# Performance work log

Hardware: AMD Instinct MI355X
Metric: run time of the kernel (lower is better)

Reference implementation:

```python
import jax, jax.numpy as jnp
import numpy as np

NUM_HEADS = 4
HIDDEN = 256
HEAD_DIM = HIDDEN // NUM_HEADS
N_NODES = 8192
N_EDGES = 262144
NEG = -1e9


def setup_inputs() -> dict:
    key = jax.random.key(0)
    ks = jax.random.split(key, 10)
    s = 1.0 / np.sqrt(HIDDEN)
    inp = {
        "node_features": jax.random.normal(ks[0], (N_NODES, HIDDEN), dtype=jnp.float32),
        "Wq": jax.random.uniform(ks[1], (HIDDEN, HIDDEN), jnp.float32, -s, s),
        "bq": jnp.zeros((HIDDEN,), jnp.float32),
        "Wk": jax.random.uniform(ks[2], (HIDDEN, HIDDEN), jnp.float32, -s, s),
        "bk": jnp.zeros((HIDDEN,), jnp.float32),
        "Wv": jax.random.uniform(ks[3], (HIDDEN, HIDDEN), jnp.float32, -s, s),
        "bv": jnp.zeros((HIDDEN,), jnp.float32),
        "Wo": jax.random.uniform(ks[4], (HIDDEN, HIDDEN), jnp.float32, -s, s),
        "bo": jnp.zeros((HIDDEN,), jnp.float32),
        "edge_index": jax.random.randint(ks[5], (2, N_EDGES), 0, N_NODES, dtype=jnp.int64),
    }
    return inp


def reference(node_features, Wq, bq, Wk, bk, Wv, bv, Wo, bo, edge_index):
    N = node_features.shape[0]
    # QKV projections -> [H, N, d]
    q = (node_features @ Wq + bq).reshape(N, NUM_HEADS, HEAD_DIM).transpose(1, 0, 2)
    k = (node_features @ Wk + bk).reshape(N, NUM_HEADS, HEAD_DIM).transpose(1, 0, 2)
    v = (node_features @ Wv + bv).reshape(N, NUM_HEADS, HEAD_DIM).transpose(1, 0, 2)
    # dense scores [H, N, N]
    scores = jnp.einsum('hnd,hmd->hnm', q, k) / jnp.sqrt(jnp.float32(HEAD_DIM))
    mask = jnp.full((N, N), NEG, dtype=jnp.float32).at[edge_index[0], edge_index[1]].set(0.0)
    scores = scores + mask[None, :, :]
    weights = jax.nn.softmax(scores, axis=-1)  # dropout is identity in eval
    context = jnp.einsum('hnm,hmd->hnd', weights, v)
    context = context.transpose(1, 0, 2).reshape(N, HIDDEN)
    return context @ Wo + bo
```

## Files before the change

### kernel.cpp

```cpp
#include <hip/hip_runtime.h>
#include <hip/hip_fp16.h>
#include <stdint.h>

#define NN 8192
#define HID 256
#define NH 4
#define HD 64
#define NE 262144
#define WPR (NN / 32)
#define CAP 128
#define NQKV 768

typedef __attribute__((ext_vector_type(8))) short s16x8;
typedef __attribute__((ext_vector_type(4))) float f32x4;
typedef _Float16 f16x2 __attribute__((ext_vector_type(2)));

__device__ __forceinline__ float fdot2(f16x2 a, f16x2 b, float c) {
#if __has_builtin(__builtin_amdgcn_fdot2)
    return __builtin_amdgcn_fdot2(a, b, c, false);
#else
    return c + (float)a.x * (float)b.x + (float)a.y * (float)b.y;
#endif
}

__device__ __forceinline__ void gload_lds16(const unsigned short* g, unsigned short* l) {
    __builtin_amdgcn_global_load_lds(
        (const __attribute__((address_space(1))) unsigned int*)g,
        (__attribute__((address_space(3))) unsigned int*)l, 16, 0, 0);
}

__global__ __launch_bounds__(256) void zero_kernel(uint4* __restrict__ p)
{
    p[blockIdx.x * 256 + threadIdx.x] = make_uint4(0, 0, 0, 0);
}

__global__ __launch_bounds__(256) void prep_kernel(
    const float* __restrict__ X,
    const float* __restrict__ Wq, const float* __restrict__ Wk,
    const float* __restrict__ Wv, const float* __restrict__ Wo,
    const float* __restrict__ bq, const float* __restrict__ bk,
    const float* __restrict__ bv, const int* __restrict__ ei,
    uint32_t* __restrict__ bitmap, unsigned short* __restrict__ Xh,
    unsigned short* __restrict__ W2Tq, unsigned short* __restrict__ W2To,
    float* __restrict__ biasq)
{
    const int b = blockIdx.x, tid = threadIdx.x;
    if (b < 1024) {
        int e = b * 256 + tid;
        int r = ei[e];
        int c = ei[NE + e];
        atomicOr(&bitmap[(size_t)r * WPR + (c >> 5)], 1u << (c & 31));
    } else if (b < 3072) {
        int i4 = ((b - 1024) * 256 + tid) * 4;
        float4 x = *(const float4*)(X + i4);
        __half2 h0 = __floats2half2_rn(x.x, x.y);
        __half2 h1 = __floats2half2_rn(x.z, x.w);
        uint2 w;
        w.x = *(unsigned*)&h0;
        w.y = *(unsigned*)&h1;
        *(uint2*)(Xh + i4) = w;
    } else {
        int lin = (b - 3072) * 256 + tid;
        int n = lin >> 8, k = lin & 255;
        const float* W; int ns; unsigned short* dst;
        if (n < NQKV) {
            W  = (n < 256) ? Wq : (n < 512) ? Wk : Wv;
            ns = n & 255;
            dst = W2Tq + (size_t)n * HID + k;
            if (k == 0) {
                const float* bsrc = (n < 256) ? bq : (n < 512) ? bk : bv;
                biasq[n] = bsrc[ns];
            }
        } else {
            W = Wo; ns = n - NQKV;
            dst = W2To + (size_t)ns * HID + k;
        }
        __half h = __float2half(W[(size_t)k * HID + ns]);
        *dst = *(unsigned short*)&h;
    }
}

template<int BN, bool HALF_OUT>
__global__ __launch_bounds__(256) void mfma_gemm_kernel(
    const unsigned short* __restrict__ A, const unsigned short* __restrict__ BT,
    const float* __restrict__ bias, void* __restrict__ Cv, int N)
{
    constexpr int NFR = BN / 32;
    __shared__ __align__(16) unsigned short Alds[128 * 32];
    __shared__ __align__(16) unsigned short Blds[BN * 32];

    const int tid  = threadIdx.x;
    const int lane = tid & 63, wave = tid >> 6;
    const int wm = wave >> 1, wn = wave & 1;

    const int nwg = gridDim.x;
    const int orig = blockIdx.x;
    const int q8 = nwg >> 3;
    const int id = (orig & 7) * q8 + (orig >> 3);
    const int m0 = (id & 63) * 128;
    const int n0 = (id >> 6) * BN;

    const int r0 = tid >> 2, cc0 = tid & 3;
    const int r1 = (tid + 256) >> 2, cc1 = (tid + 256) & 3;

    f32x4 acc[4][NFR];
    #pragma unroll
    for (int i = 0; i < 4; ++i)
        #pragma unroll
        for (int j = 0; j < NFR; ++j)
            acc[i][j] = (f32x4){0.f, 0.f, 0.f, 0.f};

    for (int step = 0; step < 8; ++step) {
        const int kk = step * 32;
        __syncthreads();
        gload_lds16(A + (size_t)(m0 + r0) * HID + kk + cc0 * 8, &Alds[tid * 8]);
        gload_lds16(A + (size_t)(m0 + r1) * HID + kk + cc1 * 8, &Alds[(tid + 256) * 8]);
        gload_lds16(BT + (size_t)(n0 + r0) * HID + kk + cc0 * 8, &Blds[tid * 8]);
        if constexpr (BN == 128)
            gload_lds16(BT + (size_t)(n0 + r1) * HID + kk + cc1 * 8, &Blds[(tid + 256) * 8]);
        __syncthreads();

        s16x8 af[4], bfr[NFR];
        #pragma unroll
        for (int i = 0; i < 4; ++i)
            af[i] = *(const s16x8*)&Alds[(wm * 64 + i * 16 + (lane & 15)) * 32 + (lane >> 4) * 8];
        #pragma unroll
        for (int j = 0; j < NFR; ++j)
            bfr[j] = *(const s16x8*)&Blds[(wn * (BN / 2) + j * 16 + (lane & 15)) * 32 + (lane >> 4) * 8];
        #pragma unroll
        for (int i = 0; i < 4; ++i)
            #pragma unroll
            for (int j = 0; j < NFR; ++j)
                acc[i][j] = __builtin_amdgcn_mfma_f32_16x16x32_f16(af[i], bfr[j], acc[i][j], 0, 0, 0);
    }

    #pragma unroll
    for (int i = 0; i < 4; ++i) {
        #pragma unroll
        for (int j = 0; j < NFR; ++j) {
            int gcol = n0 + wn * (BN / 2) + j * 16 + (lane & 15);
            float bb = bias[gcol];
            #pragma unroll
            for (int r = 0; r < 4; ++r) {
                int grow = m0 + wm * 64 + i * 16 + (lane >> 4) * 4 + r;
                float v = acc[i][j][r] + bb;
                if constexpr (HALF_OUT)
                    ((__half*)Cv)[(size_t)grow * N + gcol] = __float2half(v);
                else
                    ((float*)Cv)[(size_t)grow * N + gcol] = v;
            }
        }
    }
}

__global__ __launch_bounds__(256) void build_csr_kernel(
    const uint32_t* __restrict__ bitmap, int* __restrict__ nbr, int* __restrict__ cnt)
{
    const int row = blockIdx.x * 4 + (threadIdx.x >> 6);
    const int lane = threadIdx.x & 63;
    const uint32_t* rp = bitmap + (size_t)row * WPR + lane * 4;
    uint32_t w0 = rp[0], w1 = rp[1], w2 = rp[2], w3 = rp[3];
    int pc = __popc(w0) + __popc(w1) + __popc(w2) + __popc(w3);
    int scan = pc;
    #pragma unroll
    for (int off = 1; off < 64; off <<= 1) {
        int t = __shfl_up(scan, off);
        if (lane >= off) scan += t;
    }
    int idx = scan - pc;
    int* dst = nbr + (size_t)row * CAP;
    const int base = lane * 128;
    uint32_t ws4[4] = {w0, w1, w2, w3};
    #pragma unroll
    for (int i = 0; i < 4; ++i) {
        uint32_t w = ws4[i];
        int cb = base + i * 32;
        while (w) {
            int b = __ffs(w) - 1;
            if (idx < CAP) dst[idx] = cb + b;
            ++idx;
            w &= w - 1;
        }
    }
    if (lane == 63) cnt[row] = min(scan, CAP);
}

__global__ __launch_bounds__(256) void attn_kernel(
    const __half* __restrict__ QKV, const int* __restrict__ nbr,
    const int* __restrict__ cntg, __half* __restrict__ ctx)
{
    const int row  = blockIdx.x * 4 + (threadIdx.x >> 6);
    const int lane = threadIdx.x & 63;
    const int cnt  = cntg[row];

    uint2 qraw = ((const uint2*)(QKV + (size_t)row * NQKV))[lane];
    union { uint2 u2; f16x2 h[2]; } uq; uq.u2 = qraw;
    const f16x2 q2a = uq.h[0], q2b = uq.h[1];

    float m = -INFINITY, l = 0.f;
    float a0 = 0.f, a1 = 0.f, a2 = 0.f, a3 = 0.f;

    for (int j0 = 0; j0 < cnt; j0 += 64) {
        int mynb = (j0 + lane < cnt) ? nbr[(size_t)row * CAP + j0 + lane] : 0;
        const int nb = min(64, cnt - j0);
        for (int b = 0; b < nb; b += 8) {
            int idx[8];
            #pragma unroll
            for (int u = 0; u < 8; ++u) idx[u] = __shfl(mynb, b + u);
            uint2 kv[8], vv[8];
            #pragma unroll
            for (int u = 0; u < 8; ++u) {
                const __half* base = QKV + (size_t)idx[u] * NQKV;
                kv[u] = ((const uint2*)(base + 256))[lane];
                vv[u] = ((const uint2*)(base + 512))[lane];
            }
            float s[8];
            #pragma unroll
            for (int u = 0; u < 8; ++u) {
                union { uint2 u2; f16x2 h[2]; } uk; uk.u2 = kv[u];
                float p = fdot2(q2a, uk.h[0], 0.f);
                p = fdot2(q2b, uk.h[1], p);
                #pragma unroll
                for (int off = 1; off < 16; off <<= 1) p += __shfl_xor(p, off);
                s[u] = (b + u < nb) ? p * 0.125f : -INFINITY;
            }
            float bm = s[0];
            #pragma unroll
            for (int u = 1; u < 8; ++u) bm = fmaxf(bm, s[u]);
            float mn = fmaxf(m, bm);
            float sc = expf(m - mn);
            a0 *= sc; a1 *= sc; a2 *= sc; a3 *= sc; l *= sc;
            #pragma unroll
            for (int u = 0; u < 8; ++u) {
                float w = expf(s[u] - mn);
                l += w;
                union { uint2 u2; __half2 h[2]; } uv; uv.u2 = vv[u];
                float2 f0 = __half22float2(uv.h[0]);
                float2 f1 = __half22float2(uv.h[1]);
                a0 = fmaf(w, f0.x, a0); a1 = fmaf(w, f0.y, a1);
                a2 = fmaf(w, f1.x, a2); a3 = fmaf(w, f1.y, a3);
            }
            m = mn;
        }
    }

    uint2 outw = make_uint2(0u, 0u);
    if (cnt > 0) {
        float rl = 1.f / l;
        __half2 o0 = __floats2half2_rn(a0 * rl, a1 * rl);
        __half2 o1 = __floats2half2_rn(a2 * rl, a3 * rl);
        outw.x = *(unsigned*)&o0;
        outw.y = *(unsigned*)&o1;
    }
    ((uint2*)(ctx + (size_t)row * HID))[lane] = outw;
}

extern "C" void kernel_launch(void* const* d_in, const int* in_sizes, int n_in,
                              void* d_out, int out_size, void* d_ws, size_t ws_size,
                              hipStream_t stream)
{
    const float* X  = (const float*)d_in[0];
    const float* Wq = (const float*)d_in[1];
    const float* bq = (const float*)d_in[2];
    const float* Wk = (const float*)d_in[3];
    const float* bk = (const float*)d_in[4];
    const float* Wv = (const float*)d_in[5];
    const float* bv = (const float*)d_in[6];
    const float* Wo = (const float*)d_in[7];
    const float* bo = (const float*)d_in[8];
    const int*   ei = (const int*)d_in[9];
    float* out = (float*)d_out;

    char* ws = (char*)d_ws;
    __half*         QKV    = (__half*)ws;
    uint32_t*       bitmap = (uint32_t*)ws;
    unsigned short* Xh     = (unsigned short*)(ws + 16777216);
    __half*         ctx    = (__half*)Xh;
    unsigned short* W2Tq   = (unsigned short*)(ws + 20971520);
    unsigned short* W2To   = (unsigned short*)(ws + 21364736);
    float*          biasq  = (float*)(ws + 21495808);
    int*            nbrL   = (int*)(ws + 21498880);
    int*            cntL   = (int*)(ws + 25693184);

    zero_kernel<<<2048, 256, 0, stream>>>((uint4*)bitmap);
    prep_kernel<<<4096, 256, 0, stream>>>(
        X, Wq, Wk, Wv, Wo, bq, bk, bv, ei, bitmap, Xh, W2Tq, W2To, biasq);
    build_csr_kernel<<<NN / 4, 256, 0, stream>>>(bitmap, nbrL, cntL);

    mfma_gemm_kernel<128, true><<<384, 256, 0, stream>>>(
        Xh, W2Tq, biasq, QKV, NQKV);

    attn_kernel<<<NN / 4, 256, 0, stream>>>(QKV, nbrL, cntL, ctx);

    mfma_gemm_kernel<64, false><<<256, 256, 0, stream>>>(
        (const unsigned short*)ctx, W2To, bo, out, HID);
}
```

Before: 79.42 us.

## Merge QKV GEMM with CSR build, shrink GEMM tiles, double-buffer attention loads

The QKV projection GEMM and the CSR build now run as one launch: the first 1536 blocks do 64x64 GEMM tiles and the remaining blocks build neighbour lists. QKV moves to its own workspace region so it no longer aliases the bitmap. Both GEMMs switch to smaller 64x64 tiles to put more workgroups on the device. The attention loop double-buffers the gathered K/V rows so the next 8 neighbours load while the current 8 are computed. The intent is to cut launch gaps, raise occupancy and hide gather latency, at the cost of less data reuse per tile and more registers in attention.

```diff
diff --git a/kernel.cpp b/kernel.cpp
--- a/kernel.cpp
+++ b/kernel.cpp
@@ -10,6 +10,7 @@
 #define WPR (NN / 32)
 #define CAP 128
 #define NQKV 768
+#define G1B 1536
 
 typedef __attribute__((ext_vector_type(8))) short s16x8;
 typedef __attribute__((ext_vector_type(4))) float f32x4;
@@ -80,69 +81,54 @@
     }
 }
 
-template<int BN, bool HALF_OUT>
-__global__ __launch_bounds__(256) void mfma_gemm_kernel(
+template<bool HALF_OUT>
+__device__ __forceinline__ void gemm64_body(
     const unsigned short* __restrict__ A, const unsigned short* __restrict__ BT,
-    const float* __restrict__ bias, void* __restrict__ Cv, int N)
-{
-    constexpr int NFR = BN / 32;
-    __shared__ __align__(16) unsigned short Alds[128 * 32];
-    __shared__ __align__(16) unsigned short Blds[BN * 32];
-
+    const float* __restrict__ bias, void* __restrict__ Cv, int N,
+    int m0, int n0, unsigned short* Alds, unsigned short* Blds)
+{
     const int tid  = threadIdx.x;
     const int lane = tid & 63, wave = tid >> 6;
     const int wm = wave >> 1, wn = wave & 1;
-
-    const int nwg = gridDim.x;
-    const int orig = blockIdx.x;
-    const int q8 = nwg >> 3;
-    const int id = (orig & 7) * q8 + (orig >> 3);
-    const int m0 = (id & 63) * 128;
-    const int n0 = (id >> 6) * BN;
-
     const int r0 = tid >> 2, cc0 = tid & 3;
-    const int r1 = (tid + 256) >> 2, cc1 = (tid + 256) & 3;
-
-    f32x4 acc[4][NFR];
+
+    f32x4 acc[2][2];
     #pragma unroll
-    for (int i = 0; i < 4; ++i)
-        #pragma unroll
-        for (int j = 0; j < NFR; ++j)
+    for (int i = 0; i < 2; ++i)
+        #pragma unroll
+        for (int j = 0; j < 2; ++j)
             acc[i][j] = (f32x4){0.f, 0.f, 0.f, 0.f};
 
     for (int step = 0; step < 8; ++step) {
         const int kk = step * 32;
         __syncthreads();
         gload_lds16(A + (size_t)(m0 + r0) * HID + kk + cc0 * 8, &Alds[tid * 8]);
-        gload_lds16(A + (size_t)(m0 + r1) * HID + kk + cc1 * 8, &Alds[(tid + 256) * 8]);
         gload_lds16(BT + (size_t)(n0 + r0) * HID + kk + cc0 * 8, &Blds[tid * 8]);
-        if constexpr (BN == 128)
-            gload_lds16(BT + (size_t)(n0 + r1) * HID + kk + cc1 * 8, &Blds[(tid + 256) * 8]);
         __syncthreads();
 
-        s16x8 af[4], bfr[NFR];
-        #pragma unroll
-        for (int i = 0; i < 4; ++i)
-            af[i] = *(const s16x8*)&Alds[(wm * 64 + i * 16 + (lane & 15)) * 32 + (lane >> 4) * 8];
-        #pragma unroll
-        for (int j = 0; j < NFR; ++j)
-            bfr[j] = *(const s16x8*)&Blds[(wn * (BN / 2) + j * 16 + (lane & 15)) * 32 + (lane >> 4) * 8];
-        #pragma unroll
-        for (int i = 0; i < 4; ++i)
-            #pragma unroll
-            for (int j = 0; j < NFR; ++j)
+        s16x8 af[2], bfr[2];
+        #pragma unroll
+        for (int i = 0; i < 2; ++i)
+            af[i] = *(const s16x8*)&Alds[(wm * 32 + i * 16 + (lane & 15)) * 32 + (lane >> 4) * 8];
+        #pragma unroll
+        for (int j = 0; j < 2; ++j)
+            bfr[j] = *(const s16x8*)&Blds[(wn * 32 + j * 16 + (lane & 15)) * 32 + (lane >> 4) * 8];
+        #pragma unroll
+        for (int i = 0; i < 2; ++i)
+            #pragma unroll
+            for (int j = 0; j < 2; ++j)
                 acc[i][j] = __builtin_amdgcn_mfma_f32_16x16x32_f16(af[i], bfr[j], acc[i][j], 0, 0, 0);
     }
 
     #pragma unroll
-    for (int i = 0; i < 4; ++i) {
-        #pragma unroll
-        for (int j = 0; j < NFR; ++j) {
-            int gcol = n0 + wn * (BN / 2) + j * 16 + (lane & 15);
+    for (int i = 0; i < 2; ++i) {
+        #pragma unroll
+        for (int j = 0; j < 2; ++j) {
+            int gcol = n0 + wn * 32 + j * 16 + (lane & 15);
             float bb = bias[gcol];
             #pragma unroll
-            for (int r = 0; r < 4; ++r) {
-                int grow = m0 + wm * 64 + i * 16 + (lane >> 4) * 4 + r;
+            for (int r = 0; r < 2 * 2; ++r) {
+                int grow = m0 + wm * 32 + i * 16 + (lane >> 4) * 4 + r;
                 float v = acc[i][j][r] + bb;
                 if constexpr (HALF_OUT)
                     ((__half*)Cv)[(size_t)grow * N + gcol] = __float2half(v);
@@ -153,10 +139,23 @@
     }
 }
 
-__global__ __launch_bounds__(256) void build_csr_kernel(
+__global__ __launch_bounds__(256) void gemm_csr_kernel(
+    const unsigned short* __restrict__ Xh, const unsigned short* __restrict__ W2Tq,
+    const float* __restrict__ biasq, __half* __restrict__ QKV,
     const uint32_t* __restrict__ bitmap, int* __restrict__ nbr, int* __restrict__ cnt)
 {
-    const int row = blockIdx.x * 4 + (threadIdx.x >> 6);
+    __shared__ __align__(16) unsigned short Alds[64 * 32];
+    __shared__ __align__(16) unsigned short Blds[64 * 32];
+
+    if (blockIdx.x < G1B) {
+        constexpr int q8 = G1B >> 3;
+        const int orig = blockIdx.x;
+        const int id = (orig & 7) * q8 + (orig >> 3);
+        gemm64_body<true>(Xh, W2Tq, biasq, QKV, NQKV,
+                          (id & 127) * 64, (id >> 7) * 64, Alds, Blds);
+        return;
+    }
+    const int row = (blockIdx.x - G1B) * 4 + (threadIdx.x >> 6);
     const int lane = threadIdx.x & 63;
     const uint32_t* rp = bitmap + (size_t)row * WPR + lane * 4;
     uint32_t w0 = rp[0], w1 = rp[1], w2 = rp[2], w3 = rp[3];
@@ -185,6 +184,19 @@
     if (lane == 63) cnt[row] = min(scan, CAP);
 }
 
+template<bool HALF_OUT>
+__global__ __launch_bounds__(256) void gemm64_kernel(
+    const unsigned short* __restrict__ A, const unsigned short* __restrict__ BT,
+    const float* __restrict__ bias, void* __restrict__ Cv, int N)
+{
+    __shared__ __align__(16) unsigned short Alds[64 * 32];
+    __shared__ __align__(16) unsigned short Blds[64 * 32];
+    const int nwg = gridDim.x, orig = blockIdx.x, q8 = nwg >> 3;
+    const int id = (orig & 7) * q8 + (orig >> 3);
+    gemm64_body<HALF_OUT>(A, BT, bias, Cv, N,
+                          (id & 127) * 64, (id >> 7) * 64, Alds, Blds);
+}
+
 __global__ __launch_bounds__(256) void attn_kernel(
     const __half* __restrict__ QKV, const int* __restrict__ nbr,
     const int* __restrict__ cntg, __half* __restrict__ ctx)
@@ -203,17 +215,19 @@
     for (int j0 = 0; j0 < cnt; j0 += 64) {
         int mynb = (j0 + lane < cnt) ? nbr[(size_t)row * CAP + j0 + lane] : 0;
         const int nb = min(64, cnt - j0);
-        for (int b = 0; b < nb; b += 8) {
-            int idx[8];
-            #pragma unroll
-            for (int u = 0; u < 8; ++u) idx[u] = __shfl(mynb, b + u);
-            uint2 kv[8], vv[8];
+
+        uint2 kvA[8], vvA[8], kvB[8], vvB[8];
+
+        auto load8 = [&](uint2* kv, uint2* vv, int bb) {
             #pragma unroll
             for (int u = 0; u < 8; ++u) {
-                const __half* base = QKV + (size_t)idx[u] * NQKV;
+                int id8 = __shfl(mynb, bb + u);
+                const __half* base = QKV + (size_t)id8 * NQKV;
                 kv[u] = ((const uint2*)(base + 256))[lane];
                 vv[u] = ((const uint2*)(base + 512))[lane];
             }
+        };
+        auto comp8 = [&](const uint2* kv, const uint2* vv, int bb) {
             float s[8];
             #pragma unroll
             for (int u = 0; u < 8; ++u) {
@@ -222,7 +236,7 @@
                 p = fdot2(q2b, uk.h[1], p);
                 #pragma unroll
                 for (int off = 1; off < 16; off <<= 1) p += __shfl_xor(p, off);
-                s[u] = (b + u < nb) ? p * 0.125f : -INFINITY;
+                s[u] = (bb + u < nb) ? p * 0.125f : -INFINITY;
             }
             float bm = s[0];
             #pragma unroll
@@ -241,6 +255,14 @@
                 a2 = fmaf(w, f1.x, a2); a3 = fmaf(w, f1.y, a3);
             }
             m = mn;
+        };
+
+        load8(kvA, vvA, 0);
+        for (int b = 0; b < nb; b += 16) {
+            if (b + 8 < nb) load8(kvB, vvB, b + 8);
+            comp8(kvA, vvA, b);
+            if (b + 16 < nb) load8(kvA, vvA, b + 16);
+            if (b + 8 < nb) comp8(kvB, vvB, b + 8);
         }
     }
 
@@ -272,26 +294,22 @@
     float* out = (float*)d_out;
 
     char* ws = (char*)d_ws;
-    __half*         QKV    = (__half*)ws;
     uint32_t*       bitmap = (uint32_t*)ws;
-    unsigned short* Xh     = (unsigned short*)(ws + 16777216);
+    __half*         QKV    = (__half*)(ws + 8388608);
+    unsigned short* Xh     = (unsigned short*)(ws + 20971520);
     __half*         ctx    = (__half*)Xh;
-    unsigned short* W2Tq   = (unsigned short*)(ws + 20971520);
-    unsigned short* W2To   = (unsigned short*)(ws + 21364736);
-    float*          biasq  = (float*)(ws + 21495808);
-    int*            nbrL   = (int*)(ws + 21498880);
-    int*            cntL   = (int*)(ws + 25693184);
+    unsigned short* W2Tq   = (unsigned short*)(ws + 25165824);
+    unsigned short* W2To   = (unsigned short*)(ws + 25559040);
+    float*          biasq  = (float*)(ws + 25690112);
+    int*            nbrL   = (int*)(ws + 25693184);
+    int*            cntL   = (int*)(ws + 29887488);
 
     zero_kernel<<<2048, 256, 0, stream>>>((uint4*)bitmap);
     prep_kernel<<<4096, 256, 0, stream>>>(
         X, Wq, Wk, Wv, Wo, bq, bk, bv, ei, bitmap, Xh, W2Tq, W2To, biasq);
-    build_csr_kernel<<<NN / 4, 256, 0, stream>>>(bitmap, nbrL, cntL);
-
-    mfma_gemm_kernel<128, true><<<384, 256, 0, stream>>>(
-        Xh, W2Tq, biasq, QKV, NQKV);
-
+    gemm_csr_kernel<<<G1B + 2048, 256, 0, stream>>>(
+        Xh, W2Tq, biasq, QKV, bitmap, nbrL, cntL);
     attn_kernel<<<NN / 4, 256, 0, stream>>>(QKV, nbrL, cntL, ctx);
-
-    mfma_gemm_kernel<64, false><<<256, 256, 0, stream>>>(
+    gemm64_kernel<false><<<512, 256, 0, stream>>>(
         (const unsigned short*)ctx, W2To, bo, out, HID);
 }
```

Result: slower. 81.82 us (+3.0%).

## Fuse QKV GEMM and CSR build into one launch via block-range dispatch

Applied to the files above, without the earlier changes.

Merges the QKV projection GEMM and the bitmap-to-CSR conversion into a single kernel: the first 384 blocks run the GEMM tile body and the remaining 2048 blocks build neighbour lists. This removes one launch and lets the two independent stages run concurrently on the GPU instead of back-to-back. The workspace is relaid out so QKV no longer aliases the bitmap, which both stages now read or write at once. CSR blocks now carry the GEMM's LDS allocation, which may lower their occupancy.

```diff
diff --git a/kernel.cpp b/kernel.cpp
--- a/kernel.cpp
+++ b/kernel.cpp
@@ -10,6 +10,7 @@
 #define WPR (NN / 32)
 #define CAP 128
 #define NQKV 768
+#define G1B 384
 
 typedef __attribute__((ext_vector_type(8))) short s16x8;
 typedef __attribute__((ext_vector_type(4))) float f32x4;
@@ -81,24 +82,15 @@
 }
 
 template<int BN, bool HALF_OUT>
-__global__ __launch_bounds__(256) void mfma_gemm_kernel(
+__device__ __forceinline__ void gemm_body(
     const unsigned short* __restrict__ A, const unsigned short* __restrict__ BT,
-    const float* __restrict__ bias, void* __restrict__ Cv, int N)
+    const float* __restrict__ bias, void* __restrict__ Cv, int N,
+    int m0, int n0, unsigned short* Alds, unsigned short* Blds)
 {
     constexpr int NFR = BN / 32;
-    __shared__ __align__(16) unsigned short Alds[128 * 32];
-    __shared__ __align__(16) unsigned short Blds[BN * 32];
-
     const int tid  = threadIdx.x;
     const int lane = tid & 63, wave = tid >> 6;
     const int wm = wave >> 1, wn = wave & 1;
-
-    const int nwg = gridDim.x;
-    const int orig = blockIdx.x;
-    const int q8 = nwg >> 3;
-    const int id = (orig & 7) * q8 + (orig >> 3);
-    const int m0 = (id & 63) * 128;
-    const int n0 = (id >> 6) * BN;
 
     const int r0 = tid >> 2, cc0 = tid & 3;
     const int r1 = (tid + 256) >> 2, cc1 = (tid + 256) & 3;
@@ -153,10 +145,23 @@
     }
 }
 
-__global__ __launch_bounds__(256) void build_csr_kernel(
+__global__ __launch_bounds__(256) void gemm_csr_kernel(
+    const unsigned short* __restrict__ Xh, const unsigned short* __restrict__ W2Tq,
+    const float* __restrict__ biasq, __half* __restrict__ QKV,
     const uint32_t* __restrict__ bitmap, int* __restrict__ nbr, int* __restrict__ cnt)
 {
-    const int row = blockIdx.x * 4 + (threadIdx.x >> 6);
+    __shared__ __align__(16) unsigned short Alds[128 * 32];
+    __shared__ __align__(16) unsigned short Blds[128 * 32];
+
+    if (blockIdx.x < G1B) {
+        constexpr int q8 = G1B >> 3;
+        const int orig = blockIdx.x;
+        const int id = (orig & 7) * q8 + (orig >> 3);
+        gemm_body<128, true>(Xh, W2Tq, biasq, QKV, NQKV,
+                             (id & 63) * 128, (id >> 6) * 128, Alds, Blds);
+        return;
+    }
+    const int row = (blockIdx.x - G1B) * 4 + (threadIdx.x >> 6);
     const int lane = threadIdx.x & 63;
     const uint32_t* rp = bitmap + (size_t)row * WPR + lane * 4;
     uint32_t w0 = rp[0], w1 = rp[1], w2 = rp[2], w3 = rp[3];
@@ -185,6 +190,19 @@
     if (lane == 63) cnt[row] = min(scan, CAP);
 }
 
+template<int BN, bool HALF_OUT>
+__global__ __launch_bounds__(256) void gemm_kernel(
+    const unsigned short* __restrict__ A, const unsigned short* __restrict__ BT,
+    const float* __restrict__ bias, void* __restrict__ Cv, int N)
+{
+    __shared__ __align__(16) unsigned short Alds[128 * 32];
+    __shared__ __align__(16) unsigned short Blds[BN * 32];
+    const int nwg = gridDim.x, orig = blockIdx.x, q8 = nwg >> 3;
+    const int id = (orig & 7) * q8 + (orig >> 3);
+    gemm_body<BN, HALF_OUT>(A, BT, bias, Cv, N,
+                            (id & 63) * 128, (id >> 6) * BN, Alds, Blds);
+}
+
 __global__ __launch_bounds__(256) void attn_kernel(
     const __half* __restrict__ QKV, const int* __restrict__ nbr,
     const int* __restrict__ cntg, __half* __restrict__ ctx)
@@ -272,26 +290,22 @@
     float* out = (float*)d_out;
 
     char* ws = (char*)d_ws;
-    __half*         QKV    = (__half*)ws;
     uint32_t*       bitmap = (uint32_t*)ws;
-    unsigned short* Xh     = (unsigned short*)(ws + 16777216);
+    __half*         QKV    = (__half*)(ws + 8388608);
+    unsigned short* Xh     = (unsigned short*)(ws + 20971520);
     __half*         ctx    = (__half*)Xh;
-    unsigned short* W2Tq   = (unsigned short*)(ws + 20971520);
-    unsigned short* W2To   = (unsigned short*)(ws + 21364736);
-    float*          biasq  = (float*)(ws + 21495808);
-    int*            nbrL   = (int*)(ws + 21498880);
-    int*            cntL   = (int*)(ws + 25693184);
+    unsigned short* W2Tq   = (unsigned short*)(ws + 25165824);
+    unsigned short* W2To   = (unsigned short*)(ws + 25559040);
+    float*          biasq  = (float*)(ws + 25690112);
+    int*            nbrL   = (int*)(ws + 25693184);
+    int*            cntL   = (int*)(ws + 29887488);
 
     zero_kernel<<<2048, 256, 0, stream>>>((uint4*)bitmap);
     prep_kernel<<<4096, 256, 0, stream>>>(
         X, Wq, Wk, Wv, Wo, bq, bk, bv, ei, bitmap, Xh, W2Tq, W2To, biasq);
-    build_csr_kernel<<<NN / 4, 256, 0, stream>>>(bitmap, nbrL, cntL);
-
-    mfma_gemm_kernel<128, true><<<384, 256, 0, stream>>>(
-        Xh, W2Tq, biasq, QKV, NQKV);
-
+    gemm_csr_kernel<<<G1B + 2048, 256, 0, stream>>>(
+        Xh, W2Tq, biasq, QKV, bitmap, nbrL, cntL);
     attn_kernel<<<NN / 4, 256, 0, stream>>>(QKV, nbrL, cntL, ctx);
-
-    mfma_gemm_kernel<64, false><<<256, 256, 0, stream>>>(
+    gemm_kernel<64, false><<<256, 256, 0, stream>>>(
         (const unsigned short*)ctx, W2To, bo, out, HID);
 }
```

After: 75.76 us, median of 2. 4.6% less time.
